# Optimization experiments

Measured on AMD Instinct MI355X. Metric: run time of the kernel, lower is better.

## Reference

```python
import jax, jax.numpy as jnp
import numpy as np

EPS = 1e-6
NEG_INF = jnp.finfo(jnp.float32).min


def setup_inputs() -> dict:
    key = jax.random.key(0)
    ks = jax.random.split(key, 12)
    N, D, H, dh, F, V, L, B = 4, 1024, 16, 64, 4096, 32000, 2048, 1
    s = 0.02
    return {
        "x_BL": jax.random.randint(ks[0], (B, L), 0, V, dtype=jnp.int32),
        "embed": jax.random.normal(ks[1], (V, D), jnp.float32) * s,
        "pos_embed": jax.random.normal(ks[2], (L, D), jnp.float32) * s,
        "wq": jax.random.normal(ks[3], (N, D, H, dh), jnp.float32) * s,
        "wk": jax.random.normal(ks[4], (N, D, H, dh), jnp.float32) * s,
        "wv": jax.random.normal(ks[5], (N, D, H, dh), jnp.float32) * s,
        "wo": jax.random.normal(ks[6], (N, H, dh, D), jnp.float32) * s,
        "gate_w": jax.random.normal(ks[7], (N, D, F), jnp.float32) * s,
        "val_w": jax.random.normal(ks[8], (N, D, F), jnp.float32) * s,
        "ffn_out_w": jax.random.normal(ks[9], (N, F, D), jnp.float32) * s,
        "ln1_s": jnp.ones((N, D), jnp.float32),
        "ln2_s": jnp.ones((N, D), jnp.float32),
        "final_ln_s": jnp.ones((D,), jnp.float32),
    }


def rmsnorm(x, scale):
    var = jnp.mean(jnp.square(x), axis=-1, keepdims=True)
    return x * jax.lax.rsqrt(var + EPS) * scale


def attention(x_BLD, wq, wk, wv, wo):
    # wq/wk/wv: [D,H,dh]; wo: [H,dh,D]
    q = jnp.einsum('bld,dhk->blhk', x_BLD, wq)
    k = jnp.einsum('bld,dhk->blhk', x_BLD, wk)
    v = jnp.einsum('bld,dhk->blhk', x_BLD, wv)
    dh = wq.shape[-1]
    a = jnp.einsum('bqhd,bkhd->bhqk', q, k) / (dh ** 0.5)
    L = x_BLD.shape[1]
    mask = jnp.tril(jnp.ones((1, 1, L, L), dtype=jnp.bool_))
    a = jnp.where(mask, a, NEG_INF)
    a = jax.nn.softmax(a, axis=-1)
    o = jnp.einsum('bhqk,bkhd->bqhd', a, v)
    return jnp.einsum('bqhd,hdD->bqD', o, wo)


def ffn(x_BLD, gate_w, val_w, out_w):
    g = jax.nn.swish(jnp.einsum('bld,df->blf', x_BLD, gate_w))
    y = jnp.einsum('bld,df->blf', x_BLD, val_w) * g
    return jnp.einsum('blf,fd->bld', y, out_w)


def reference(x_BL, embed, pos_embed, wq, wk, wv, wo, gate_w, val_w,
              ffn_out_w, ln1_s, ln2_s, final_ln_s):
    x = embed[x_BL]                              # [B,L,D]
    L = x_BL.shape[1]
    x = x + pos_embed[jnp.arange(L)][None, :, :]
    N = wq.shape[0]
    for i in range(N):
        a = attention(rmsnorm(x, ln1_s[i]), wq[i], wk[i], wv[i], wo[i])
        f = ffn(rmsnorm(x, ln2_s[i]), gate_w[i], val_w[i], ffn_out_w[i])
        x = x + a + f
    x = rmsnorm(x, final_ln_s)
    logits = jnp.einsum('bld,vd->blv', x, embed)  # tied embedding attend
    return logits
```

## Files before the change

kernel.cpp:

```cpp
#include <hip/hip_runtime.h>
#include <cstdint>
#include <cstddef>

#define L_SEQ 2048
#define DMODEL 1024
#define NHEAD 16
#define DHEAD 64
#define FFN_F 4096
#define VOCAB 32000
#define NLAYER 4

typedef __attribute__((ext_vector_type(8))) short short8;
typedef __attribute__((ext_vector_type(4))) float f32x4;

__device__ __forceinline__ unsigned short f2bf(float f) {
  unsigned int u = __float_as_uint(f);
  u += 0x7fffu + ((u >> 16) & 1u);
  return (unsigned short)(u >> 16);
}
__device__ __forceinline__ float b2f(unsigned short h) {
  return __uint_as_float(((unsigned int)h) << 16);
}

__device__ __forceinline__ void glds16(const unsigned short* g, unsigned short* l) {
  __builtin_amdgcn_global_load_lds(
      (const __attribute__((address_space(1))) unsigned int*)g,
      (__attribute__((address_space(3))) unsigned int*)l, 16, 0, 0);
}

__device__ __forceinline__ float rmax16(float v) {
  v = fmaxf(v, __shfl_xor(v, 1));
  v = fmaxf(v, __shfl_xor(v, 2));
  v = fmaxf(v, __shfl_xor(v, 4));
  v = fmaxf(v, __shfl_xor(v, 8));
  return v;
}
__device__ __forceinline__ float rsum16(float v) {
  v += __shfl_xor(v, 1);
  v += __shfl_xor(v, 2);
  v += __shfl_xor(v, 4);
  v += __shfl_xor(v, 8);
  return v;
}

#define MFMA(ACC, AF, BF) \
  ACC = __builtin_amdgcn_mfma_f32_16x16x32_bf16(AF, BF, ACC, 0, 0, 0)

enum { E_F32 = 0, E_BF16 = 1, E_SWIGLU = 2, E_PART = 3 };

template <int EPI>
__global__ __launch_bounds__(512, 2) void gemm8p(
    const unsigned short* __restrict__ A, const unsigned short* __restrict__ B,
    void* __restrict__ Cg, int M, int N, int K, int lda, int ldb, int ldc,
    float alpha, int nby)
{
  const int nwg = gridDim.x;
  const int orig = blockIdx.x;
  const int q = nwg >> 3, r = nwg & 7;
  const int xcd = orig & 7, rest = orig >> 3;
  const int wgid = (xcd < r ? xcd * (q + 1) : r * (q + 1) + (xcd - r) * q) + rest;
  const int by = wgid % nby, bx = wgid / nby;
  const int mb = by * 256, nb = bx * 256;

  __shared__ __align__(16) unsigned short As_[2][256 * 64];
  __shared__ __align__(16) unsigned short Bs_[2][256 * 64];

  const int tid = threadIdx.x;
  const int lane = tid & 63;
  const int w = tid >> 6;
  const int wm = (w >> 2) * 128;
  const int wn = (w & 3) * 64;
  const int lr = lane & 15;
  const int lg = lane >> 4;
  const int srow = lane >> 3;
  const int scol = ((lane & 7) ^ srow) * 8;
  const int slot0 = (lg ^ (lr & 7)) * 8;
  const int slot1 = ((4 + lg) ^ (lr & 7)) * 8;

  f32x4 acc[8][4];
#pragma unroll
  for (int i = 0; i < 8; i++)
#pragma unroll
    for (int j = 0; j < 4; j++) acc[i][j] = (f32x4){0.f, 0.f, 0.f, 0.f};

  const unsigned short* Ab = A + (size_t)(mb + srow) * lda + scol;
  const unsigned short* Bb = B + (size_t)(nb + srow) * ldb + scol;

  auto stageA = [&](int t, int R) {
    const int s = t & 1, kb = t << 6;
#pragma unroll
    for (int c = 0; c < 2; c++) {
      int cid = w * 2 + c;
      int rb = ((cid >> 3) << 7) + R * 64 + ((cid & 7) << 3);
      glds16(Ab + (size_t)rb * lda + kb, &As_[s][rb * 64]);
    }
  };
  auto stageB = [&](int t, int R) {
    const int s = t & 1, kb = t << 6;
#pragma unroll
    for (int c = 0; c < 2; c++) {
      int cid = w * 2 + c;
      int rb = ((cid >> 2) << 6) + R * 32 + ((cid & 3) << 3);
      glds16(Bb + (size_t)rb * ldb + kb, &Bs_[s][rb * 64]);
    }
  };

  const int nk = K >> 6;
  stageA(0, 0); stageA(0, 1); stageB(0, 0); stageB(0, 1);
  stageA(1, 0); stageB(1, 0); stageB(1, 1);
  asm volatile("s_waitcnt vmcnt(6)" ::: "memory");
  __builtin_amdgcn_s_barrier();

  short8 a[4][2], b0[2][2], b1[2][2];
#pragma unroll
  for (int j = 0; j < 2; j++) {
    b0[j][0] = *(const short8*)&Bs_[0][(wn + j * 16 + lr) * 64 + slot0];
    b0[j][1] = *(const short8*)&Bs_[0][(wn + j * 16 + lr) * 64 + slot1];
  }

  for (int t = 0; t < nk; ++t) {
    const int s = t & 1;
    const unsigned short* Asb = &As_[s][0];
    const unsigned short* Bsb = &Bs_[s][0];

#pragma unroll
    for (int i = 0; i < 4; i++) {
      a[i][0] = *(const short8*)&Asb[(wm + i * 16 + lr) * 64 + slot0];
      a[i][1] = *(const short8*)&Asb[(wm + i * 16 + lr) * 64 + slot1];
    }
    if (t + 1 < nk) stageA(t + 1, 1);
    __builtin_amdgcn_s_barrier();
    __builtin_amdgcn_s_setprio(1);
#pragma unroll
    for (int kk = 0; kk < 2; kk++)
#pragma unroll
      for (int i = 0; i < 4; i++)
#pragma unroll
        for (int j = 0; j < 2; j++) MFMA(acc[i][j], a[i][kk], b0[j][kk]);
    __builtin_amdgcn_s_setprio(0);
    __builtin_amdgcn_s_barrier();

#pragma unroll
    for (int j = 0; j < 2; j++) {
      b1[j][0] = *(const short8*)&Bsb[(wn + 32 + j * 16 + lr) * 64 + slot0];
      b1[j][1] = *(const short8*)&Bsb[(wn + 32 + j * 16 + lr) * 64 + slot1];
    }
    if (t + 2 < nk) stageA(t + 2, 0);
    __builtin_amdgcn_s_barrier();
    __builtin_amdgcn_s_setprio(1);
#pragma unroll
    for (int kk = 0; kk < 2; kk++)
#pragma unroll
      for (int i = 0; i < 4; i++)
#pragma unroll
        for (int j = 0; j < 2; j++) MFMA(acc[i][2 + j], a[i][kk], b1[j][kk]);
    __builtin_amdgcn_s_setprio(0);
    __builtin_amdgcn_s_barrier();

#pragma unroll
    for (int i = 0; i < 4; i++) {
      a[i][0] = *(const short8*)&Asb[(wm + 64 + i * 16 + lr) * 64 + slot0];
      a[i][1] = *(const short8*)&Asb[(wm + 64 + i * 16 + lr) * 64 + slot1];
    }
    if (t + 2 < nk) stageB(t + 2, 0);
    __builtin_amdgcn_s_barrier();
    __builtin_amdgcn_s_setprio(1);
#pragma unroll
    for (int kk = 0; kk < 2; kk++)
#pragma unroll
      for (int i = 0; i < 4; i++)
#pragma unroll
        for (int j = 0; j < 2; j++) MFMA(acc[4 + i][2 + j], a[i][kk], b1[j][kk]);
    __builtin_amdgcn_s_setprio(0);
    __builtin_amdgcn_s_barrier();

    if (t + 2 < nk) stageB(t + 2, 1);
    __builtin_amdgcn_s_barrier();
    __builtin_amdgcn_s_setprio(1);
#pragma unroll
    for (int kk = 0; kk < 2; kk++)
#pragma unroll
      for (int i = 0; i < 4; i++)
#pragma unroll
        for (int j = 0; j < 2; j++) MFMA(acc[4 + i][j], a[i][kk], b0[j][kk]);
    __builtin_amdgcn_s_setprio(0);
    if (t + 2 < nk) {
      asm volatile("s_waitcnt vmcnt(6)" ::: "memory");
    } else {
      asm volatile("s_waitcnt vmcnt(0)" ::: "memory");
    }
    __builtin_amdgcn_s_barrier();
    if (t + 1 < nk) {
      const unsigned short* Bn = &Bs_[s ^ 1][0];
#pragma unroll
      for (int j = 0; j < 2; j++) {
        b0[j][0] = *(const short8*)&Bn[(wn + j * 16 + lr) * 64 + slot0];
        b0[j][1] = *(const short8*)&Bn[(wn + j * 16 + lr) * 64 + slot1];
      }
    }
  }

#pragma unroll
  for (int i = 0; i < 8; i++) {
#pragma unroll
    for (int j = 0; j < 4; j++) {
      int oc = nb + wn + 16 * j + lr;
#pragma unroll
      for (int r4 = 0; r4 < 4; r4++) {
        int orow = mb + wm + 16 * i + lg * 4 + r4;
        float v = acc[i][j][r4] * alpha;
        if (EPI == E_F32) {
          ((float*)Cg)[(size_t)orow * ldc + oc] = v;
        } else if (EPI == E_BF16) {
          ((unsigned short*)Cg)[(size_t)orow * ldc + oc] = f2bf(v);
        } else if (EPI == E_SWIGLU) {
          float other = __shfl_xor(v, 1);
          float g = (lane & 1) ? other : v;
          float vv = (lane & 1) ? v : other;
          float sw = g / (1.0f + expf(-g)) * vv;
          if (!(lane & 1))
            ((unsigned short*)Cg)[(size_t)orow * ldc + (oc >> 1)] = f2bf(sw);
        }
      }
    }
  }
}

template <int EPI>
__global__ __launch_bounds__(256) void gemm_fast(
    const unsigned short* __restrict__ A, const unsigned short* __restrict__ B,
    void* __restrict__ Cg, int M, int N, int K, int lda, int ldb, int ldc,
    float alpha, int nbx)
{
  const int nwg = gridDim.x;
  const int orig = blockIdx.x;
  const int q = nwg >> 3, r = nwg & 7;
  const int xcd = orig & 7, rest = orig >> 3;
  const int wgid = (xcd < r ? xcd * (q + 1) : r * (q + 1) + (xcd - r) * q) + rest;
  const int bx = wgid % nbx, by = wgid / nbx;
  const int mb = by * 128;
  const int nb = bx * 128;

  const int Keff = (EPI == E_PART) ? (K >> 2) : K;
  const int koff = (EPI == E_PART) ? blockIdx.z * Keff : 0;

  __shared__ __align__(16) unsigned short As[2][128 * 64];
  __shared__ __align__(16) unsigned short Bs[2][128 * 64];

  const int tid = threadIdx.x;
  const int lane = tid & 63;
  const int wave = tid >> 6;
  const int wm = (wave >> 1) * 64;
  const int wn = (wave & 1) * 64;
  const int lr = lane & 15;
  const int lg = lane >> 4;

  const int srow = lane >> 3;
  const int scol = ((lane & 7) ^ srow) * 8;

  f32x4 acc[4][4];
#pragma unroll
  for (int i = 0; i < 4; i++)
#pragma unroll
    for (int j = 0; j < 4; j++) acc[i][j] = (f32x4){0.f, 0.f, 0.f, 0.f};

  const unsigned short* Abase = A + (size_t)(mb + wave * 32 + srow) * lda + koff + scol;
  const unsigned short* Bbase = B + (size_t)(nb + wave * 32 + srow) * ldb + koff + scol;

  auto stage = [&](int kb, int b) {
#pragma unroll
    for (int c = 0; c < 4; c++)
      glds16(Abase + (size_t)(c * 8) * lda + kb, &As[b][(wave * 32 + c * 8) * 64]);
#pragma unroll
    for (int c = 0; c < 4; c++)
      glds16(Bbase + (size_t)(c * 8) * ldb + kb, &Bs[b][(wave * 32 + c * 8) * 64]);
  };

  stage(0, 0);
  __syncthreads();
  int cur = 0;
  const int nk = Keff >> 6;

  for (int t = 0; t < nk; ++t) {
    if (t + 1 < nk) stage((t + 1) << 6, cur ^ 1);

    short8 af[2][4], bfb[2][4];
#pragma unroll
    for (int h = 0; h < 2; h++) {
      const int swz = ((h * 4 + lg) ^ (lr & 7)) * 8;
#pragma unroll
      for (int i = 0; i < 4; i++) {
        af[h][i] = *(const short8*)&As[cur][(wm + 16 * i + lr) * 64 + swz];
        bfb[h][i] = *(const short8*)&Bs[cur][(wn + 16 * i + lr) * 64 + swz];
      }
    }
#pragma unroll
    for (int h = 0; h < 2; h++)
#pragma unroll
      for (int i = 0; i < 4; i++)
#pragma unroll
        for (int j = 0; j < 4; j++) MFMA(acc[i][j], af[h][i], bfb[h][j]);

    __syncthreads();
    cur ^= 1;
  }

#pragma unroll
  for (int i = 0; i < 4; i++) {
#pragma unroll
    for (int j = 0; j < 4; j++) {
      int oc = nb + wn + 16 * j + lr;
#pragma unroll
      for (int r4 = 0; r4 < 4; r4++) {
        int orow = mb + wm + 16 * i + lg * 4 + r4;
        float v = acc[i][j][r4] * alpha;
        if (EPI == E_F32) {
          ((float*)Cg)[(size_t)orow * ldc + oc] = v;
        } else if (EPI == E_BF16) {
          ((unsigned short*)Cg)[(size_t)orow * ldc + oc] = f2bf(v);
        } else {
          float* C = (float*)Cg + (size_t)blockIdx.z * ((size_t)L_SEQ * DMODEL);
          C[(size_t)orow * ldc + oc] = v;
        }
      }
    }
  }
}

__global__ __launch_bounds__(128) void flash_attn(
    const unsigned short* __restrict__ Qg, const unsigned short* __restrict__ Kg,
    const unsigned short* __restrict__ Vt, unsigned short* __restrict__ Og,
    int ldq, int ldo)
{
  const int bid = blockIdx.x;
  const int slot = bid & 255, ph = bid >> 8;
  const int h = slot >> 4;
  const int qs = slot & 15;
  const int qb = ph ? (31 - qs) : qs;

  const int tid = threadIdx.x;
  const int lane = tid & 63;
  const int w = tid >> 6;
  const int lr = lane & 15;
  const int lg = lane >> 4;

  __shared__ __align__(16) unsigned short KsL[2][64 * 64];
  __shared__ __align__(16) unsigned short VsL[2][64 * 64];
  __shared__ __align__(16) unsigned short Ps[2][32 * 64];

  const int srow = lane >> 3;
  const int scol = ((lane & 7) ^ srow) * 8;

  short8 qf[2][2];
#pragma unroll
  for (int i = 0; i < 2; i++)
#pragma unroll
    for (int kk = 0; kk < 2; kk++)
      qf[i][kk] = *(const short8*)(Qg +
          (size_t)(qb * 64 + w * 32 + i * 16 + lr) * ldq + h * 64 + kk * 32 + lg * 8);

  f32x4 acc_o[2][4];
  float m_st[2][4], l_st[2][4];
#pragma unroll
  for (int i = 0; i < 2; i++)
#pragma unroll
    for (int j = 0; j < 4; j++) acc_o[i][j] = (f32x4){0.f, 0.f, 0.f, 0.f};
#pragma unroll
  for (int i = 0; i < 2; i++)
#pragma unroll
    for (int r = 0; r < 4; r++) { m_st[i][r] = -1e30f; l_st[i][r] = 0.f; }

  const int ntiles = qb + 1;
  const int qmin = qb * 64 + w * 32;

  auto stage = [&](int t, int buf) {
#pragma unroll
    for (int c = 0; c < 4; c++) {
      int row = w * 32 + c * 8 + srow;
      glds16(Kg + (size_t)(t * 64 + row) * ldq + h * 64 + scol,
             &KsL[buf][row * 64]);
      glds16(Vt + (size_t)(h * 64 + row) * L_SEQ + t * 64 + scol,
             &VsL[buf][row * 64]);
    }
  };

  stage(0, 0);
  __syncthreads();
  int buf = 0;

  for (int t = 0; t < ntiles; t++) {
    if (t + 1 < ntiles) stage(t + 1, buf ^ 1);

    f32x4 sa[2][4];
#pragma unroll
    for (int i = 0; i < 2; i++)
#pragma unroll
      for (int j = 0; j < 4; j++) sa[i][j] = (f32x4){0.f, 0.f, 0.f, 0.f};
#pragma unroll
    for (int kk = 0; kk < 2; kk++) {
      short8 kf[4];
#pragma unroll
      for (int j = 0; j < 4; j++)
        kf[j] = *(const short8*)&KsL[buf][(j * 16 + lr) * 64 + ((kk * 4 + lg) ^ (lr & 7)) * 8];
#pragma unroll
      for (int i = 0; i < 2; i++)
#pragma unroll
        for (int j = 0; j < 4; j++) MFMA(sa[i][j], qf[i][kk], kf[j]);
    }

    const bool diag = (t * 64 + 63) > qmin;
#pragma unroll
    for (int i = 0; i < 2; i++)
#pragma unroll
      for (int j = 0; j < 4; j++)
#pragma unroll
        for (int r = 0; r < 4; r++) {
          float s = sa[i][j][r] * 0.125f;
          if (diag) {
            int kg = t * 64 + j * 16 + lr;
            int qg = qmin + i * 16 + lg * 4 + r;
            if (kg > qg) s = -1e30f;
          }
          sa[i][j][r] = s;
        }

    float fsc[2][4], mnew[2][4];
#pragma unroll
    for (int i = 0; i < 2; i++)
#pragma unroll
      for (int r = 0; r < 4; r++) {
        float mx = fmaxf(fmaxf(sa[i][0][r], sa[i][1][r]), fmaxf(sa[i][2][r], sa[i][3][r]));
        mx = rmax16(mx);
        float mn = fmaxf(m_st[i][r], mx);
        mnew[i][r] = mn;
        fsc[i][r] = __expf(m_st[i][r] - mn);
        m_st[i][r] = mn;
      }
#pragma unroll
    for (int i = 0; i < 2; i++)
#pragma unroll
      for (int r = 0; r < 4; r++) {
        float ls = 0.f;
#pragma unroll
        for (int j = 0; j < 4; j++) {
          float p = __expf(sa[i][j][r] - mnew[i][r]);
          sa[i][j][r] = p;
          ls += p;
        }
        ls = rsum16(ls);
        l_st[i][r] = l_st[i][r] * fsc[i][r] + ls;
      }
#pragma unroll
    for (int i = 0; i < 2; i++)
#pragma unroll
      for (int j = 0; j < 4; j++)
#pragma unroll
        for (int r = 0; r < 4; r++) acc_o[i][j][r] *= fsc[i][r];

#pragma unroll
    for (int i = 0; i < 2; i++)
#pragma unroll
      for (int j = 0; j < 4; j++)
#pragma unroll
        for (int r = 0; r < 4; r++) {
          int qrl = lg * 4 + r;
          int idx = (i * 16 + qrl) * 64 + (((j * 2 + (lr >> 3)) ^ (qrl & 7)) * 8) + (lr & 7);
          Ps[w][idx] = f2bf(sa[i][j][r]);
        }

#pragma unroll
    for (int kk = 0; kk < 2; kk++) {
      short8 pf[2], vf[4];
#pragma unroll
      for (int i = 0; i < 2; i++)
        pf[i] = *(const short8*)&Ps[w][(i * 16 + lr) * 64 + ((kk * 4 + lg) ^ (lr & 7)) * 8];
#pragma unroll
      for (int j = 0; j < 4; j++)
        vf[j] = *(const short8*)&VsL[buf][(j * 16 + lr) * 64 + ((kk * 4 + lg) ^ (lr & 7)) * 8];
#pragma unroll
      for (int i = 0; i < 2; i++)
#pragma unroll
        for (int j = 0; j < 4; j++) MFMA(acc_o[i][j], pf[i], vf[j]);
    }

    __syncthreads();
    buf ^= 1;
  }

  float inv[2][4];
#pragma unroll
  for (int i = 0; i < 2; i++)
#pragma unroll
    for (int r = 0; r < 4; r++) inv[i][r] = 1.0f / l_st[i][r];
#pragma unroll
  for (int i = 0; i < 2; i++)
#pragma unroll
    for (int j = 0; j < 4; j++)
#pragma unroll
      for (int r = 0; r < 4; r++) {
        size_t row = qmin + i * 16 + lg * 4 + r;
        Og[row * ldo + h * 64 + j * 16 + lr] = f2bf(acc_o[i][j][r] * inv[i][r]);
      }
}

__global__ __launch_bounds__(256) void rmsnorm_fold(
    const float* __restrict__ xin, const float* __restrict__ pb,
    unsigned short* __restrict__ o1, float* __restrict__ xout, int fold)
{
  int row = blockIdx.x;
  int tid = threadIdx.x;
  const size_t SL = (size_t)L_SEQ * DMODEL;
  float v[4];
  float ss = 0.f;
#pragma unroll
  for (int i = 0; i < 4; i++) {
    size_t idx = (size_t)row * DMODEL + tid + 256 * i;
    float val = xin[idx];
    if (fold) {
      val += pb[idx] + pb[idx + SL] + pb[idx + 2 * SL] + pb[idx + 3 * SL];
      xout[idx] = val;
    }
    v[i] = val;
    ss += val * val;
  }
#pragma unroll
  for (int o = 32; o > 0; o >>= 1) ss += __shfl_xor(ss, o);
  __shared__ float red[4];
  if ((tid & 63) == 0) red[tid >> 6] = ss;
  __syncthreads();
  ss = red[0] + red[1] + red[2] + red[3];
  float inv = rsqrtf(ss / DMODEL + 1e-6f);
#pragma unroll
  for (int i = 0; i < 4; i++) {
    size_t idx = (size_t)row * DMODEL + tid + 256 * i;
    o1[idx] = f2bf(v[i] * inv);
  }
}

__global__ __launch_bounds__(256) void prep_weights(
    const float* __restrict__ wq, const float* __restrict__ wk,
    const float* __restrict__ wv, const float* __restrict__ wo,
    const float* __restrict__ gw, const float* __restrict__ vw,
    const float* __restrict__ fw, const float* __restrict__ s1,
    const float* __restrict__ s2,
    unsigned short* __restrict__ qkvw, unsigned short* __restrict__ wft,
    unsigned short* __restrict__ gvt)
{
  __shared__ float t0[32][33], t1[32][33];
  int bid = blockIdx.x;
  int tx = threadIdx.x, ty = threadIdx.y;
  if (bid < 4096) {
    int j = bid >> 10, tile = bid & 1023;
    int c0 = (tile & 31) * 32, r0 = (tile >> 5) * 32;
    const float* src = j == 0 ? wq : j == 1 ? wk : j == 2 ? wv : wo;
#pragma unroll
    for (int k = 0; k < 32; k += 8)
      t0[ty + k][tx] = src[(size_t)(r0 + ty + k) * 1024 + c0 + tx];
    __syncthreads();
    if (j < 3) {
      unsigned short* dst = qkvw + (size_t)j * 1024 * 1024;
      float sc = s1[r0 + tx];
#pragma unroll
      for (int k = 0; k < 32; k += 8)
        dst[(size_t)(c0 + ty + k) * 1024 + r0 + tx] = f2bf(t0[tx][ty + k] * sc);
    } else {
#pragma unroll
      for (int k = 0; k < 32; k += 8)
        wft[(size_t)(c0 + ty + k) * 5120 + r0 + tx] = f2bf(t0[tx][ty + k]);
    }
  } else if (bid < 8192) {
    int tile = bid - 4096;
    int c0 = (tile & 31) * 32;
    int r0 = (tile >> 5) * 32;
#pragma unroll
    for (int k = 0; k < 32; k += 8)
      t0[ty + k][tx] = fw[(size_t)(r0 + ty + k) * 1024 + c0 + tx];
    __syncthreads();
#pragma unroll
    for (int k = 0; k < 32; k += 8)
      wft[(size_t)(c0 + ty + k) * 5120 + 1024 + r0 + tx] = f2bf(t0[tx][ty + k]);
  } else {
    int tile = bid - 8192;
    int c0 = (tile & 127) * 32;
    int d0 = (tile >> 7) * 32;
#pragma unroll
    for (int k = 0; k < 32; k += 8) {
      t0[ty + k][tx] = gw[(size_t)(d0 + ty + k) * 4096 + c0 + tx];
      t1[ty + k][tx] = vw[(size_t)(d0 + ty + k) * 4096 + c0 + tx];
    }
    __syncthreads();
    float sc = s2[d0 + tx];
#pragma unroll
    for (int k = 0; k < 32; k += 8) {
      gvt[(size_t)(2 * (c0 + ty + k)) * 1024 + d0 + tx] = f2bf(t0[tx][ty + k] * sc);
      gvt[(size_t)(2 * (c0 + ty + k) + 1) * 1024 + d0 + tx] = f2bf(t1[tx][ty + k] * sc);
    }
  }
}

__global__ __launch_bounds__(256) void transpose_act(
    const unsigned short* __restrict__ in, unsigned short* __restrict__ out,
    int ld_in, int ld_out)
{
  __shared__ unsigned short tile[32][33];
  int c0 = blockIdx.x * 32;
  int r0 = blockIdx.y * 32;
  int tx = threadIdx.x;
  int ty = threadIdx.y;
#pragma unroll
  for (int j = 0; j < 32; j += 8)
    tile[ty + j][tx] = in[(size_t)(r0 + ty + j) * ld_in + c0 + tx];
  __syncthreads();
#pragma unroll
  for (int j = 0; j < 32; j += 8)
    out[(size_t)(c0 + ty + j) * ld_out + r0 + tx] = tile[tx][ty + j];
}

__global__ __launch_bounds__(256) void convert_embb(
    const float* __restrict__ in, const float* __restrict__ lnf,
    unsigned short* __restrict__ out, size_t n)
{
  size_t i = ((size_t)blockIdx.x * 256 + threadIdx.x) * 4;
  if (i + 3 < n) {
    float4 v = *(const float4*)(in + i);
    int d = (int)(i & 1023);
    out[i] = f2bf(v.x * lnf[d]);
    out[i + 1] = f2bf(v.y * lnf[d + 1]);
    out[i + 2] = f2bf(v.z * lnf[d + 2]);
    out[i + 3] = f2bf(v.w * lnf[d + 3]);
  }
}

__global__ __launch_bounds__(256) void embed_kernel(
    const int* __restrict__ ids, const float* __restrict__ emb,
    const float* __restrict__ pos, float* __restrict__ x)
{
  int l = blockIdx.x;
  int id = ids[l];
#pragma unroll
  for (int i = 0; i < 4; i++) {
    int d = threadIdx.x + 256 * i;
    x[(size_t)l * DMODEL + d] = emb[(size_t)id * DMODEL + d] + pos[(size_t)l * DMODEL + d];
  }
}

extern "C" void kernel_launch(void* const* d_in, const int* in_sizes, int n_in,
                              void* d_out, int out_size, void* d_ws, size_t ws_size,
                              hipStream_t stream)
{
  const int L = L_SEQ, D = DMODEL, F = FFN_F, V = VOCAB;
  const int* ids = (const int*)d_in[0];
  const float* embed = (const float*)d_in[1];
  const float* pos = (const float*)d_in[2];
  const float* wq = (const float*)d_in[3];
  const float* wk = (const float*)d_in[4];
  const float* wv = (const float*)d_in[5];
  const float* wo = (const float*)d_in[6];
  const float* gatew = (const float*)d_in[7];
  const float* valw = (const float*)d_in[8];
  const float* ffow = (const float*)d_in[9];
  const float* ln1 = (const float*)d_in[10];
  const float* ln2 = (const float*)d_in[11];
  const float* lnf = (const float*)d_in[12];

  char* ws = (char*)d_ws;
  size_t off = 0;
  auto alloc = [&](size_t bytes) -> void* {
    void* p = ws + off;
    off += (bytes + 255) & ~(size_t)255;
    return p;
  };
  float* x = (float*)alloc((size_t)L * D * 4);
  float* pbuf = (float*)alloc((size_t)4 * L * D * 4);
  unsigned short* xhat = (unsigned short*)alloc((size_t)L * D * 2);
  unsigned short* qkvb = (unsigned short*)alloc((size_t)L * 3 * D * 2);
  unsigned short* vtb = (unsigned short*)alloc((size_t)L * D * 2);
  unsigned short* ohb = (unsigned short*)alloc((size_t)L * 5120 * 2);
  unsigned short* qkvw = (unsigned short*)alloc((size_t)3 * D * D * 2);
  unsigned short* gvt = (unsigned short*)alloc((size_t)2 * F * D * 2);
  unsigned short* wft = (unsigned short*)alloc((size_t)D * 5120 * 2);
  unsigned short* embb = (unsigned short*)alloc((size_t)V * D * 2);

  dim3 blk(256);
  dim3 blk512(512);
  dim3 blkT(32, 8);

  embed_kernel<<<L, blk, 0, stream>>>(ids, embed, pos, x);
  convert_embb<<<(unsigned)((size_t)V * D / 1024), blk, 0, stream>>>(
      embed, lnf, embb, (size_t)V * D);

  for (int i = 0; i < NLAYER; i++) {
    prep_weights<<<12288, blkT, 0, stream>>>(
        wq + (size_t)i * D * D, wk + (size_t)i * D * D, wv + (size_t)i * D * D,
        wo + (size_t)i * D * D, gatew + (size_t)i * D * F, valw + (size_t)i * D * F,
        ffow + (size_t)i * F * D, ln1 + (size_t)i * D, ln2 + (size_t)i * D,
        qkvw, wft, gvt);

    rmsnorm_fold<<<L, blk, 0, stream>>>(x, pbuf, xhat, x, i > 0 ? 1 : 0);

    gemm_fast<E_BF16><<<dim3(24 * 16), blk, 0, stream>>>(
        xhat, qkvw, qkvb, L, 3 * D, D, D, D, 3 * D, 1.0f, 24);

    transpose_act<<<dim3(D / 32, L / 32), blkT, 0, stream>>>(qkvb + 2 * D, vtb, 3 * D, L);

    flash_attn<<<dim3(512), dim3(128), 0, stream>>>(qkvb, qkvb + D, vtb, ohb, 3 * D, 5120);

    gemm8p<E_SWIGLU><<<dim3(8 * 32), blk512, 0, stream>>>(
        xhat, gvt, ohb + 1024, L, 2 * F, D, D, D, 5120, 1.0f, 8);

    gemm_fast<E_PART><<<dim3(8 * 16, 1, 4), blk, 0, stream>>>(
        ohb, wft, pbuf, L, D, 5120, 5120, 5120, D, 1.0f, 8);
  }

  rmsnorm_fold<<<L, blk, 0, stream>>>(x, pbuf, xhat, x, 1);
  gemm8p<E_F32><<<dim3(8 * 125), blk512, 0, stream>>>(
      xhat, embb, d_out, L, V, D, D, D, V, 1.0f, 8);
}
```

Before: 1.114 ms.

## Fuse V transpose into QKV GEMM by computing V^T directly

Replaces the QKV GEMM plus separate transpose kernel with one GEMM kernel. Its first 256 workgroups compute Q and K into a [L,2D] buffer, and the remaining 128 compute V^T = Wv·xhat^T directly into the transposed layout that flash attention reads. This drops one kernel launch and the extra read and write of V per layer. The new kernel hard-codes a stride of 2048, which fits both outputs (2D for QK, L for V^T), and remaps workgroups across XCDs.

```diff
diff --git a/kernel.cpp b/kernel.cpp
--- a/kernel.cpp
+++ b/kernel.cpp
@@ -327,6 +327,104 @@
   }
 }
 
+__global__ __launch_bounds__(256) void gemm_qkv(
+    const unsigned short* __restrict__ xhat, const unsigned short* __restrict__ qkvw,
+    unsigned short* __restrict__ qkb, unsigned short* __restrict__ vtb)
+{
+  const int nwg = gridDim.x;
+  const int orig = blockIdx.x;
+  const int q = nwg >> 3, r = nwg & 7;
+  const int xcd = orig & 7, rest = orig >> 3;
+  const int wgid = (xcd < r ? xcd * (q + 1) : r * (q + 1) + (xcd - r) * q) + rest;
+
+  const unsigned short *A, *B;
+  unsigned short* C;
+  int mb, nb;
+  if (wgid < 256) {
+    mb = (wgid & 15) * 128;
+    nb = (wgid >> 4) * 128;
+    A = xhat; B = qkvw; C = qkb;
+  } else {
+    int id = wgid - 256;
+    mb = (id & 7) * 128;
+    nb = (id >> 3) * 128;
+    A = qkvw + (size_t)2 * DMODEL * DMODEL; B = xhat; C = vtb;
+  }
+
+  __shared__ __align__(16) unsigned short As[2][128 * 64];
+  __shared__ __align__(16) unsigned short Bs[2][128 * 64];
+
+  const int tid = threadIdx.x;
+  const int lane = tid & 63;
+  const int wave = tid >> 6;
+  const int wm = (wave >> 1) * 64;
+  const int wn = (wave & 1) * 64;
+  const int lr = lane & 15;
+  const int lg = lane >> 4;
+  const int srow = lane >> 3;
+  const int scol = ((lane & 7) ^ srow) * 8;
+
+  f32x4 acc[4][4];
+#pragma unroll
+  for (int i = 0; i < 4; i++)
+#pragma unroll
+    for (int j = 0; j < 4; j++) acc[i][j] = (f32x4){0.f, 0.f, 0.f, 0.f};
+
+  const unsigned short* Abase = A + (size_t)(mb + wave * 32 + srow) * DMODEL + scol;
+  const unsigned short* Bbase = B + (size_t)(nb + wave * 32 + srow) * DMODEL + scol;
+
+  auto stage = [&](int kb, int b) {
+#pragma unroll
+    for (int c = 0; c < 4; c++)
+      glds16(Abase + (size_t)(c * 8) * DMODEL + kb, &As[b][(wave * 32 + c * 8) * 64]);
+#pragma unroll
+    for (int c = 0; c < 4; c++)
+      glds16(Bbase + (size_t)(c * 8) * DMODEL + kb, &Bs[b][(wave * 32 + c * 8) * 64]);
+  };
+
+  stage(0, 0);
+  __syncthreads();
+  int cur = 0;
+  const int nk = DMODEL >> 6;
+
+  for (int t = 0; t < nk; ++t) {
+    if (t + 1 < nk) stage((t + 1) << 6, cur ^ 1);
+
+    short8 af[2][4], bfb[2][4];
+#pragma unroll
+    for (int h = 0; h < 2; h++) {
+      const int swz = ((h * 4 + lg) ^ (lr & 7)) * 8;
+#pragma unroll
+      for (int i = 0; i < 4; i++) {
+        af[h][i] = *(const short8*)&As[cur][(wm + 16 * i + lr) * 64 + swz];
+        bfb[h][i] = *(const short8*)&Bs[cur][(wn + 16 * i + lr) * 64 + swz];
+      }
+    }
+#pragma unroll
+    for (int h = 0; h < 2; h++)
+#pragma unroll
+      for (int i = 0; i < 4; i++)
+#pragma unroll
+        for (int j = 0; j < 4; j++) MFMA(acc[i][j], af[h][i], bfb[h][j]);
+
+    __syncthreads();
+    cur ^= 1;
+  }
+
+#pragma unroll
+  for (int i = 0; i < 4; i++) {
+#pragma unroll
+    for (int j = 0; j < 4; j++) {
+      int oc = nb + wn + 16 * j + lr;
+#pragma unroll
+      for (int r4 = 0; r4 < 4; r4++) {
+        int orow = mb + wm + 16 * i + lg * 4 + r4;
+        C[(size_t)orow * 2048 + oc] = f2bf(acc[i][j][r4]);
+      }
+    }
+  }
+}
+
 __global__ __launch_bounds__(128) void flash_attn(
     const unsigned short* __restrict__ Qg, const unsigned short* __restrict__ Kg,
     const unsigned short* __restrict__ Vt, unsigned short* __restrict__ Og,
@@ -596,24 +694,6 @@
       gvt[(size_t)(2 * (c0 + ty + k) + 1) * 1024 + d0 + tx] = f2bf(t1[tx][ty + k] * sc);
     }
   }
-}
-
-__global__ __launch_bounds__(256) void transpose_act(
-    const unsigned short* __restrict__ in, unsigned short* __restrict__ out,
-    int ld_in, int ld_out)
-{
-  __shared__ unsigned short tile[32][33];
-  int c0 = blockIdx.x * 32;
-  int r0 = blockIdx.y * 32;
-  int tx = threadIdx.x;
-  int ty = threadIdx.y;
-#pragma unroll
-  for (int j = 0; j < 32; j += 8)
-    tile[ty + j][tx] = in[(size_t)(r0 + ty + j) * ld_in + c0 + tx];
-  __syncthreads();
-#pragma unroll
-  for (int j = 0; j < 32; j += 8)
-    out[(size_t)(c0 + ty + j) * ld_out + r0 + tx] = tile[tx][ty + j];
 }
 
 __global__ __launch_bounds__(256) void convert_embb(
@@ -673,8 +753,8 @@
   float* x = (float*)alloc((size_t)L * D * 4);
   float* pbuf = (float*)alloc((size_t)4 * L * D * 4);
   unsigned short* xhat = (unsigned short*)alloc((size_t)L * D * 2);
-  unsigned short* qkvb = (unsigned short*)alloc((size_t)L * 3 * D * 2);
-  unsigned short* vtb = (unsigned short*)alloc((size_t)L * D * 2);
+  unsigned short* qkb = (unsigned short*)alloc((size_t)L * 2 * D * 2);
+  unsigned short* vtb = (unsigned short*)alloc((size_t)D * L * 2);
   unsigned short* ohb = (unsigned short*)alloc((size_t)L * 5120 * 2);
   unsigned short* qkvw = (unsigned short*)alloc((size_t)3 * D * D * 2);
   unsigned short* gvt = (unsigned short*)alloc((size_t)2 * F * D * 2);
@@ -698,12 +778,9 @@
 
     rmsnorm_fold<<<L, blk, 0, stream>>>(x, pbuf, xhat, x, i > 0 ? 1 : 0);
 
-    gemm_fast<E_BF16><<<dim3(24 * 16), blk, 0, stream>>>(
-        xhat, qkvw, qkvb, L, 3 * D, D, D, D, 3 * D, 1.0f, 24);
-
-    transpose_act<<<dim3(D / 32, L / 32), blkT, 0, stream>>>(qkvb + 2 * D, vtb, 3 * D, L);
-
-    flash_attn<<<dim3(512), dim3(128), 0, stream>>>(qkvb, qkvb + D, vtb, ohb, 3 * D, 5120);
+    gemm_qkv<<<dim3(384), blk, 0, stream>>>(xhat, qkvw, qkb, vtb);
+
+    flash_attn<<<dim3(512), dim3(128), 0, stream>>>(qkb, qkb + D, vtb, ohb, 2 * D, 5120);
 
     gemm8p<E_SWIGLU><<<dim3(8 * 32), blk512, 0, stream>>>(
         xhat, gvt, ohb + 1024, L, 2 * F, D, D, D, 5120, 1.0f, 8);
```

Measured after the change: 1.118 ms, median of 3. No clear change (+0.3%).
